# Optimization experiments

Measured on AMD Instinct MI355X. Metric: run time of the kernel, lower is better.

The kernel has to match this reference:

```python
import jax, jax.numpy as jnp
import numpy as np

N = 384       # nodes
K = 60        # neighbors per node
SUB = 20      # subsample_k
C_S = 128
C_Z = 128
H = 4
D_HEAD = C_Z // H
NUM_RBF = 64
E = N * K
EPS = 1e-8


def _rbf(D, D_min=0.0, D_max=20.0, D_count=NUM_RBF):
    # radial basis expansion of distances: [..., ] -> [..., D_count]
    mu = jnp.linspace(D_min, D_max, D_count)
    sigma = (D_max - D_min) / D_count
    return jnp.exp(-(((D[..., None] - mu) / sigma) ** 2))


def setup_inputs() -> dict:
    key = jax.random.key(0)
    ks = jax.random.split(key, 16)
    f32 = jnp.float32
    inp = {
        "node_features": jax.random.normal(ks[0], (N, C_S), f32),
        "node_trans": jax.random.normal(ks[1], (N, 3), f32) * 5.0,
        "edge_features": jax.random.normal(ks[2], (E, C_Z), f32),
        "edge_index": jax.random.randint(ks[3], (2, E), 0, N),
        "subsample_idx": jax.random.randint(ks[4], (N, K, SUB), 0, K),
        # dist_bias_gate: Linear(2*c_s -> H)
        "W_gate": jax.random.normal(ks[5], (2 * C_S, H), f32) / np.sqrt(2 * C_S),
        "b_gate": jnp.zeros((H,), f32),
        # dist_bias: Linear(num_rbf -> H)
        "W_db": jax.random.normal(ks[6], (NUM_RBF, H), f32) / np.sqrt(NUM_RBF),
        "b_db": jnp.zeros((H,), f32),
        # lin_qk: Linear(c_z -> 2*c_z)
        "W_qk": jax.random.normal(ks[7], (C_Z, 2 * C_Z), f32) / np.sqrt(C_Z),
        "b_qk": jnp.zeros((2 * C_Z,), f32),
        # lin_v: Linear(c_z -> c_z)
        "W_v": jax.random.normal(ks[8], (C_Z, C_Z), f32) / np.sqrt(C_Z),
        "b_v": jnp.zeros((C_Z,), f32),
        # lin_out: Linear(c_z -> c_z) (init='final' in source; random here for testing)
        "W_out": jax.random.normal(ks[9], (C_Z, C_Z), f32) / np.sqrt(C_Z),
        "b_out": jnp.zeros((C_Z,), f32),
    }
    return inp


def reference(node_features, node_trans, edge_features, edge_index, subsample_idx,
              W_gate, b_gate, W_db, b_db, W_qk, b_qk, W_v, b_v, W_out, b_out):
    n, k, sub = subsample_idx.shape
    # assume_sorted=True path: edges are grouped k-per-destination-node
    dst = edge_index[0].reshape(n, k)                           # [n,k] neighbor ids
    edge1 = jnp.broadcast_to(dst[:, :, None], (n, k, sub))      # [n,k,sub]
    edge2 = jnp.take_along_axis(
        jnp.broadcast_to(dst[:, None, :], (n, k, k)), subsample_idx, axis=-1)  # [n,k,sub]

    f1 = node_features[edge1]                                   # [n,k,sub,c_s]
    f2 = node_features[edge2]
    gate = jax.nn.sigmoid(jnp.concatenate([f1, f2], axis=-1) @ W_gate + b_gate)  # [n,k,sub,H]

    t1 = node_trans[edge1]                                      # [n,k,sub,3]
    t2 = node_trans[edge2]
    dist = jnp.linalg.norm(t1 - t2 + EPS, axis=-1)              # [n,k,sub]
    bias = gate * (_rbf(dist) @ W_db + b_db)                    # [n,k,sub,H]

    edges = edge_features.reshape(n, k, C_Z)
    qk = edges @ W_qk + b_qk
    q, kk = jnp.split(qk, 2, axis=-1)
    q = q.reshape(n, k, H, D_HEAD)
    kk = kk.reshape(n, k, H, D_HEAD)

    batch = jnp.arange(n)[:, None, None]
    k_sub = kk[batch, subsample_idx]                            # [n,k,sub,H,d]
    attn = jnp.einsum('nkhd,nkshd->nksh', q, k_sub) / np.sqrt(C_Z) + bias
    attn = jax.nn.softmax(attn, axis=2)                         # softmax over subsample axis

    v = (edges @ W_v + b_v).reshape(n, k, H, D_HEAD)
    v_sub = v[batch, subsample_idx]                             # [n,k,sub,H,d]
    upd = jnp.einsum('nksh,nkshd->nkhd', attn, v_sub).reshape(n * k, C_Z)
    return upd @ W_out + b_out                                  # [E, c_z]
```

## Files before the change

kernel.cpp:

```cpp
#include <hip/hip_runtime.h>
#include <hip/hip_bf16.h>

typedef unsigned short ushortT;
typedef __attribute__((ext_vector_type(8))) short bf16x8;
typedef __attribute__((ext_vector_type(4))) float f32x4;

#define N_NODES 384
#define KNBR 60
#define SUBK 20
#define NEDGE (N_NODES * KNBR)
#define EPSC 1e-8f
#define INV_SQRT_CZ 0.08838834764831845f
#define MU_STEP (20.0f / 63.0f)
#define INV_MU_STEP (63.0f / 20.0f)
#define INV_SIGMA 3.2f

__device__ __forceinline__ float bflo(unsigned int u) { return __uint_as_float(u << 16); }
__device__ __forceinline__ float bfhi(unsigned int u) { return __uint_as_float(u & 0xffff0000u); }
__device__ __forceinline__ ushortT f2bu(float v) {
  union { float f; unsigned int u; } c;
  c.f = v;
  return (ushortT)((c.u + 0x7fffu + ((c.u >> 16) & 1u)) >> 16);
}
__device__ __forceinline__ unsigned int pack2bf(float x, float y) {
  return (unsigned int)f2bu(x) | ((unsigned int)f2bu(y) << 16);
}
__device__ __forceinline__ ushortT f2h(float x) {
  _Float16 h = (_Float16)x;
  return __builtin_bit_cast(ushortT, h);
}
__device__ __forceinline__ float h2f(ushortT u) {
  return (float)__builtin_bit_cast(_Float16, u);
}

__global__ __launch_bounds__(256) void prep_kernel(
    const float* __restrict__ nf, const float* __restrict__ Wg, float* __restrict__ g,
    const float* __restrict__ Wqk, const float* __restrict__ bqk,
    const float* __restrict__ Wv, const float* __restrict__ bv,
    const float* __restrict__ Wout,
    ushortT* __restrict__ Wp1, ushortT* __restrict__ Wp2, float* __restrict__ bc) {
  int b = blockIdx.x, tid = threadIdx.x;
  if (b < 96) {
    int n = b * 4 + (tid >> 6), t = tid & 63;
    float a = nf[n * 128 + t];
    float bb = nf[n * 128 + 64 + t];
    float acc[8];
#pragma unroll
    for (int h = 0; h < 4; ++h) {
      acc[h]     = a * Wg[t * 4 + h]         + bb * Wg[(t + 64) * 4 + h];
      acc[4 + h] = a * Wg[(128 + t) * 4 + h] + bb * Wg[(192 + t) * 4 + h];
    }
#pragma unroll
    for (int i = 0; i < 8; ++i)
#pragma unroll
      for (int off = 32; off >= 1; off >>= 1) acc[i] += __shfl_xor(acc[i], off, 64);
    if (t == 0) {
#pragma unroll
      for (int i = 0; i < 8; ++i) g[n * 8 + i] = acc[i];
    }
  } else {
    int i = (b - 96) * 256 + tid;
    if (i < 49152) {
      int j = i & 7, l = (i >> 3) & 63, t = (i >> 9) & 3;
      int nt = (i >> 11) % 12, ny = (i >> 11) / 12;
      int nn = ny * 192 + nt * 16 + (l & 15);
      int k = t * 32 + (l >> 4) * 8 + j;
      float v = (nn < 256) ? Wqk[k * 256 + nn] : Wv[k * 128 + (nn - 256)];
      if (nn < 128) v *= INV_SQRT_CZ;
      Wp1[i] = f2bu(v);
    } else {
      int i2 = i - 49152;
      int j = i2 & 7, l = (i2 >> 3) & 63, t = (i2 >> 9) & 3, nt = (i2 >> 11);
      int nn = nt * 16 + (l & 15);
      int k = t * 32 + (l >> 4) * 8 + j;
      Wp2[i2] = f2bu(Wout[k * 128 + nn]);
    }
    if (i < 384) {
      float v = (i < 256) ? bqk[i] : bv[i - 256];
      if (i < 128) v *= INV_SQRT_CZ;
      bc[i] = v;
    }
  }
}

__global__ __launch_bounds__(512, 4) void fused_kernel(
    const float* __restrict__ ef, const ushortT* __restrict__ Wp1,
    const ushortT* __restrict__ Wp2, const float* __restrict__ bc,
    const float* __restrict__ bout, const float* __restrict__ g,
    const float* __restrict__ node_trans, const int* __restrict__ edge_index,
    const int* __restrict__ sub_idx, const float* __restrict__ W_db,
    const float* __restrict__ b_db, const float* __restrict__ b_gate,
    float* __restrict__ outp) {
  __shared__ __align__(16) ushortT kvb[KNBR * 256];
  __shared__ __align__(16) ushortT updq[64 * 136];
  __shared__ __align__(16) ushortT biasb[KNBR * SUBK * 4];
  __shared__ ushortT sub_lds[KNBR * SUBK];
  __shared__ float trs[KNBR * 3];
  __shared__ float gg[KNBR * 8];

  int n = blockIdx.x, tid = threadIdx.x;
  int e0 = n * KNBR;
  int w = tid >> 6, l = tid & 63;
  int lr = l & 15, lc = l >> 4;
  int rowA = (w & 3) * 16 + lr;
  int rowAc = min(rowA, KNBR - 1);
  int Tbase = (tid >> 8) * 12;

  if (tid < KNBR) {
    int dst = edge_index[e0 + tid];
#pragma unroll
    for (int c = 0; c < 3; ++c) trs[tid * 3 + c] = node_trans[dst * 3 + c];
#pragma unroll
    for (int i = 0; i < 8; ++i) gg[tid * 8 + i] = g[dst * 8 + i];
  }

  bf16x8 bcur[4], bnxt[4];
#pragma unroll
  for (int t = 0; t < 4; ++t)
    bcur[t] = *(const bf16x8*)(Wp1 + ((Tbase * 4 + t) * 64 + l) * 8);

  bf16x8 afrag[4];
#pragma unroll
  for (int t = 0; t < 4; ++t) {
    const float* ap = ef + (size_t)(e0 + rowAc) * 128 + t * 32 + lc * 8;
    float4 lo = *(const float4*)ap;
    float4 hi = *(const float4*)(ap + 4);
    bf16x8 a;
    a[0] = (short)f2bu(lo.x); a[1] = (short)f2bu(lo.y);
    a[2] = (short)f2bu(lo.z); a[3] = (short)f2bu(lo.w);
    a[4] = (short)f2bu(hi.x); a[5] = (short)f2bu(hi.y);
    a[6] = (short)f2bu(hi.z); a[7] = (short)f2bu(hi.w);
    afrag[t] = a;
  }

#pragma unroll
  for (int Ti = 0; Ti < 12; ++Ti) {
    int T = Tbase + Ti;
    if (Ti < 11) {
#pragma unroll
      for (int t = 0; t < 4; ++t)
        bnxt[t] = *(const bf16x8*)(Wp1 + (((T + 1) * 4 + t) * 64 + l) * 8);
    }
    f32x4 acc = {0.f, 0.f, 0.f, 0.f};
#pragma unroll
    for (int t = 0; t < 4; ++t)
      acc = __builtin_amdgcn_mfma_f32_16x16x32_bf16(bcur[t], afrag[t], acc, 0, 0, 0);
    int col0 = T * 16 + lc * 4;
    float4 bi = *(const float4*)(bc + col0);
    float o0 = acc[0] + bi.x, o1 = acc[1] + bi.y;
    float o2 = acc[2] + bi.z, o3 = acc[3] + bi.w;
    uint2 o;
    o.x = pack2bf(o0, o1);
    o.y = pack2bf(o2, o3);
    if (T < 8) {
      *(uint2*)(updq + rowA * 136 + col0) = o;
    } else if (rowA < KNBR) {
      int colk = col0 - 128;
      int base_b = (colk & 128) << 1;
      int d = colk & 127;
      int inner = ((d >> 3) & 1) * 128 + (((d >> 4) * 16) ^ ((rowA & 7) << 4)) + (d & 7) * 2;
      *(uint2*)((char*)kvb + rowA * 512 + base_b + inner) = o;
    }
#pragma unroll
    for (int t = 0; t < 4; ++t) bcur[t] = bnxt[t];
  }
  __syncthreads();

  float4 bgv = *(const float4*)b_gate;
  float4 bdbv = *(const float4*)b_db;
  for (int p = tid; p < KNBR * SUBK; p += 512) {
    int kl = p / SUBK, s = p - kl * SUBK;
    int j = sub_idx[(size_t)(e0 + kl) * SUBK + s];
    sub_lds[p] = (ushortT)j;
    float dx = trs[kl * 3 + 0] - trs[j * 3 + 0] + EPSC;
    float dy = trs[kl * 3 + 1] - trs[j * 3 + 1] + EPSC;
    float dz = trs[kl * 3 + 2] - trs[j * 3 + 2] + EPSC;
    float dist = sqrtf(dx * dx + dy * dy + dz * dz);
    int r0 = (int)(dist * INV_MU_STEP + 0.5f);
    int rlo = max(r0 - 4, 0), rhi = min(r0 + 4, 63);
    float a0 = 0.f, a1 = 0.f, a2 = 0.f, a3 = 0.f;
    for (int r = rlo; r <= rhi; ++r) {
      float t = (dist - r * MU_STEP) * INV_SIGMA;
      float e = __expf(-t * t);
      float4 wv = ((const float4*)W_db)[r];
      a0 += e * wv.x; a1 += e * wv.y; a2 += e * wv.z; a3 += e * wv.w;
    }
    float g1 = gg[kl * 8 + 0] + gg[j * 8 + 4 + 0] + bgv.x;
    float g2 = gg[kl * 8 + 1] + gg[j * 8 + 4 + 1] + bgv.y;
    float g3 = gg[kl * 8 + 2] + gg[j * 8 + 4 + 2] + bgv.z;
    float g4 = gg[kl * 8 + 3] + gg[j * 8 + 4 + 3] + bgv.w;
    biasb[p * 4 + 0] = f2h((a0 + bdbv.x) / (1.0f + __expf(-g1)));
    biasb[p * 4 + 1] = f2h((a1 + bdbv.y) / (1.0f + __expf(-g2)));
    biasb[p * 4 + 2] = f2h((a2 + bdbv.z) / (1.0f + __expf(-g3)));
    biasb[p * 4 + 3] = f2h((a3 + bdbv.w) / (1.0f + __expf(-g4)));
  }
  __syncthreads();

  int row3 = tid >> 3, h = (tid >> 1) & 3, dh = tid & 1;
  int row3c = min(row3, KNBR - 1);
  int hdo = (h * 2 + dh) * 16;
  const char* kvbase = (const char*)kvb;
  float q0, q1, q2, q3, q4, q5, q6, q7, q8, q9, q10, q11, q12, q13, q14, q15;
  {
    const ushortT* qp = updq + row3 * 136 + h * 32 + dh * 16;
    uint4 u0 = *(const uint4*)qp;
    uint4 u1 = *(const uint4*)(qp + 8);
    q0 = bflo(u0.x); q1 = bfhi(u0.x); q2 = bflo(u0.y); q3 = bfhi(u0.y);
    q4 = bflo(u0.z); q5 = bfhi(u0.z); q6 = bflo(u0.w); q7 = bfhi(u0.w);
    q8 = bflo(u1.x); q9 = bfhi(u1.x); q10 = bflo(u1.y); q11 = bfhi(u1.y);
    q12 = bflo(u1.z); q13 = bfhi(u1.z); q14 = bflo(u1.w); q15 = bfhi(u1.w);
  }
  float den = 0.f;
  float v0 = 0.f, v1 = 0.f, v2 = 0.f, v3 = 0.f, v4 = 0.f, v5 = 0.f, v6 = 0.f, v7 = 0.f;
  float v8 = 0.f, v9 = 0.f, v10 = 0.f, v11 = 0.f, v12 = 0.f, v13 = 0.f, v14 = 0.f, v15 = 0.f;
#pragma unroll 4
  for (int s = 0; s < SUBK; ++s) {
    int j = sub_lds[row3c * SUBK + s];
    int off = hdo ^ ((j & 7) << 4);
    const char* kr = kvbase + j * 512;
    uint4 k0 = *(const uint4*)(kr + off);
    uint4 k1 = *(const uint4*)(kr + 128 + off);
    float dot = q0 * bflo(k0.x) + q1 * bfhi(k0.x) + q2 * bflo(k0.y) + q3 * bfhi(k0.y) +
                q4 * bflo(k0.z) + q5 * bfhi(k0.z) + q6 * bflo(k0.w) + q7 * bfhi(k0.w) +
                q8 * bflo(k1.x) + q9 * bfhi(k1.x) + q10 * bflo(k1.y) + q11 * bfhi(k1.y) +
                q12 * bflo(k1.z) + q13 * bfhi(k1.z) + q14 * bflo(k1.w) + q15 * bfhi(k1.w);
    dot += __shfl_xor(dot, 1);
    float p = __expf(dot + h2f(biasb[(row3c * SUBK + s) * 4 + h]));
    den += p;
    uint4 w0 = *(const uint4*)(kr + 256 + off);
    uint4 w1 = *(const uint4*)(kr + 384 + off);
    v0 += p * bflo(w0.x); v1 += p * bfhi(w0.x); v2 += p * bflo(w0.y); v3 += p * bfhi(w0.y);
    v4 += p * bflo(w0.z); v5 += p * bfhi(w0.z); v6 += p * bflo(w0.w); v7 += p * bfhi(w0.w);
    v8 += p * bflo(w1.x); v9 += p * bfhi(w1.x); v10 += p * bflo(w1.y); v11 += p * bfhi(w1.y);
    v12 += p * bflo(w1.z); v13 += p * bfhi(w1.z); v14 += p * bflo(w1.w); v15 += p * bfhi(w1.w);
  }
  float inv = 1.0f / den;
  {
    uint4 o;
    o.x = pack2bf(v0 * inv, v1 * inv);
    o.y = pack2bf(v2 * inv, v3 * inv);
    o.z = pack2bf(v4 * inv, v5 * inv);
    o.w = pack2bf(v6 * inv, v7 * inv);
    *(uint4*)(updq + row3 * 136 + h * 32 + dh * 16) = o;
    uint4 o2;
    o2.x = pack2bf(v8 * inv, v9 * inv);
    o2.y = pack2bf(v10 * inv, v11 * inv);
    o2.z = pack2bf(v12 * inv, v13 * inv);
    o2.w = pack2bf(v14 * inv, v15 * inv);
    *(uint4*)(updq + row3 * 136 + h * 32 + dh * 16 + 8) = o2;
  }
  __syncthreads();

  int T4base = (tid >> 8) * 4;
  bf16x8 af2[4];
#pragma unroll
  for (int t = 0; t < 4; ++t)
    af2[t] = *(const bf16x8*)(updq + rowA * 136 + t * 32 + lc * 8);
  bf16x8 c2[4], n2[4];
#pragma unroll
  for (int t = 0; t < 4; ++t)
    c2[t] = *(const bf16x8*)(Wp2 + ((T4base * 4 + t) * 64 + l) * 8);
#pragma unroll
  for (int Ti = 0; Ti < 4; ++Ti) {
    int T = T4base + Ti;
    if (Ti < 3) {
#pragma unroll
      for (int t = 0; t < 4; ++t)
        n2[t] = *(const bf16x8*)(Wp2 + (((T + 1) * 4 + t) * 64 + l) * 8);
    }
    f32x4 acc = {0.f, 0.f, 0.f, 0.f};
#pragma unroll
    for (int t = 0; t < 4; ++t)
      acc = __builtin_amdgcn_mfma_f32_16x16x32_bf16(c2[t], af2[t], acc, 0, 0, 0);
    if (rowA < KNBR) {
      int col0 = T * 16 + lc * 4;
      float4 bi = *(const float4*)(bout + col0);
      float4 o;
      o.x = acc[0] + bi.x; o.y = acc[1] + bi.y;
      o.z = acc[2] + bi.z; o.w = acc[3] + bi.w;
      *(float4*)(outp + (size_t)(e0 + rowA) * 128 + col0) = o;
    }
#pragma unroll
    for (int t = 0; t < 4; ++t) c2[t] = n2[t];
  }
}

extern "C" void kernel_launch(void* const* d_in, const int* in_sizes, int n_in, void* d_out,
                              int out_size, void* d_ws, size_t ws_size, hipStream_t stream) {
  const float* nf  = (const float*)d_in[0];
  const float* nt  = (const float*)d_in[1];
  const float* ef  = (const float*)d_in[2];
  const int*   ei  = (const int*)d_in[3];
  const int*   si  = (const int*)d_in[4];
  const float* Wg  = (const float*)d_in[5];
  const float* bg  = (const float*)d_in[6];
  const float* Wdb = (const float*)d_in[7];
  const float* bdb = (const float*)d_in[8];
  const float* Wqk = (const float*)d_in[9];
  const float* bqk = (const float*)d_in[10];
  const float* Wv  = (const float*)d_in[11];
  const float* bv  = (const float*)d_in[12];
  const float* Wout = (const float*)d_in[13];
  const float* bout = (const float*)d_in[14];
  float* out = (float*)d_out;

  float* g      = (float*)d_ws;
  float* bc     = g + 3072;
  ushortT* Wp1  = (ushortT*)(bc + 384);
  ushortT* Wp2  = Wp1 + 49152;

  prep_kernel<<<dim3(352), dim3(256), 0, stream>>>(nf, Wg, g, Wqk, bqk, Wv, bv, Wout,
                                                   Wp1, Wp2, bc);
  fused_kernel<<<dim3(N_NODES), dim3(512), 0, stream>>>(ef, Wp1, Wp2, bc, bout, g, nt, ei, si,
                                                        Wdb, bdb, bg, out);
}
```

Before: 40.91 us.

## Vectorize attention dot/accumulate with float2 packed math and drop staging barrier

Rewrites the per-subsample QK dot product and PV accumulation using two-wide float vectors so the compiler can emit packed FMA instructions (v_pk_fma_f32) on CDNA. Separately, it removes the shared-memory staging of neighbor translations and gate terms, and the barrier that followed the first GEMM. The bias loop now reads edge_index, node_trans and g directly from global memory. This trades an LDS stage and a barrier for redundant, cache-served global gathers.

```diff
diff --git a/kernel.cpp b/kernel.cpp
--- a/kernel.cpp
+++ b/kernel.cpp
@@ -4,6 +4,7 @@
 typedef unsigned short ushortT;
 typedef __attribute__((ext_vector_type(8))) short bf16x8;
 typedef __attribute__((ext_vector_type(4))) float f32x4;
+typedef __attribute__((ext_vector_type(2))) float f32x2;
 
 #define N_NODES 384
 #define KNBR 60
@@ -17,6 +18,12 @@
 
 __device__ __forceinline__ float bflo(unsigned int u) { return __uint_as_float(u << 16); }
 __device__ __forceinline__ float bfhi(unsigned int u) { return __uint_as_float(u & 0xffff0000u); }
+__device__ __forceinline__ f32x2 bfpair(unsigned int u) {
+  f32x2 r;
+  r.x = bflo(u);
+  r.y = bfhi(u);
+  return r;
+}
 __device__ __forceinline__ ushortT f2bu(float v) {
   union { float f; unsigned int u; } c;
   c.f = v;
@@ -95,8 +102,6 @@
   __shared__ __align__(16) ushortT updq[64 * 136];
   __shared__ __align__(16) ushortT biasb[KNBR * SUBK * 4];
   __shared__ ushortT sub_lds[KNBR * SUBK];
-  __shared__ float trs[KNBR * 3];
-  __shared__ float gg[KNBR * 8];
 
   int n = blockIdx.x, tid = threadIdx.x;
   int e0 = n * KNBR;
@@ -105,14 +110,6 @@
   int rowA = (w & 3) * 16 + lr;
   int rowAc = min(rowA, KNBR - 1);
   int Tbase = (tid >> 8) * 12;
-
-  if (tid < KNBR) {
-    int dst = edge_index[e0 + tid];
-#pragma unroll
-    for (int c = 0; c < 3; ++c) trs[tid * 3 + c] = node_trans[dst * 3 + c];
-#pragma unroll
-    for (int i = 0; i < 8; ++i) gg[tid * 8 + i] = g[dst * 8 + i];
-  }
 
   bf16x8 bcur[4], bnxt[4];
 #pragma unroll
@@ -164,7 +161,6 @@
 #pragma unroll
     for (int t = 0; t < 4; ++t) bcur[t] = bnxt[t];
   }
-  __syncthreads();
 
   float4 bgv = *(const float4*)b_gate;
   float4 bdbv = *(const float4*)b_db;
@@ -172,9 +168,11 @@
     int kl = p / SUBK, s = p - kl * SUBK;
     int j = sub_idx[(size_t)(e0 + kl) * SUBK + s];
     sub_lds[p] = (ushortT)j;
-    float dx = trs[kl * 3 + 0] - trs[j * 3 + 0] + EPSC;
-    float dy = trs[kl * 3 + 1] - trs[j * 3 + 1] + EPSC;
-    float dz = trs[kl * 3 + 2] - trs[j * 3 + 2] + EPSC;
+    int dk = edge_index[e0 + kl];
+    int dj = edge_index[e0 + j];
+    float dx = node_trans[dk * 3 + 0] - node_trans[dj * 3 + 0] + EPSC;
+    float dy = node_trans[dk * 3 + 1] - node_trans[dj * 3 + 1] + EPSC;
+    float dz = node_trans[dk * 3 + 2] - node_trans[dj * 3 + 2] + EPSC;
     float dist = sqrtf(dx * dx + dy * dy + dz * dz);
     int r0 = (int)(dist * INV_MU_STEP + 0.5f);
     int rlo = max(r0 - 4, 0), rhi = min(r0 + 4, 63);
@@ -185,10 +183,12 @@
       float4 wv = ((const float4*)W_db)[r];
       a0 += e * wv.x; a1 += e * wv.y; a2 += e * wv.z; a3 += e * wv.w;
     }
-    float g1 = gg[kl * 8 + 0] + gg[j * 8 + 4 + 0] + bgv.x;
-    float g2 = gg[kl * 8 + 1] + gg[j * 8 + 4 + 1] + bgv.y;
-    float g3 = gg[kl * 8 + 2] + gg[j * 8 + 4 + 2] + bgv.z;
-    float g4 = gg[kl * 8 + 3] + gg[j * 8 + 4 + 3] + bgv.w;
+    float4 gk = *(const float4*)(g + dk * 8);
+    float4 gj = *(const float4*)(g + dj * 8 + 4);
+    float g1 = gk.x + gj.x + bgv.x;
+    float g2 = gk.y + gj.y + bgv.y;
+    float g3 = gk.z + gj.z + bgv.z;
+    float g4 = gk.w + gj.w + bgv.w;
     biasb[p * 4 + 0] = f2h((a0 + bdbv.x) / (1.0f + __expf(-g1)));
     biasb[p * 4 + 1] = f2h((a1 + bdbv.y) / (1.0f + __expf(-g2)));
     biasb[p * 4 + 2] = f2h((a2 + bdbv.z) / (1.0f + __expf(-g3)));
@@ -200,19 +200,17 @@
   int row3c = min(row3, KNBR - 1);
   int hdo = (h * 2 + dh) * 16;
   const char* kvbase = (const char*)kvb;
-  float q0, q1, q2, q3, q4, q5, q6, q7, q8, q9, q10, q11, q12, q13, q14, q15;
+  f32x2 qv0, qv1, qv2, qv3, qv4, qv5, qv6, qv7;
   {
     const ushortT* qp = updq + row3 * 136 + h * 32 + dh * 16;
     uint4 u0 = *(const uint4*)qp;
     uint4 u1 = *(const uint4*)(qp + 8);
-    q0 = bflo(u0.x); q1 = bfhi(u0.x); q2 = bflo(u0.y); q3 = bfhi(u0.y);
-    q4 = bflo(u0.z); q5 = bfhi(u0.z); q6 = bflo(u0.w); q7 = bfhi(u0.w);
-    q8 = bflo(u1.x); q9 = bfhi(u1.x); q10 = bflo(u1.y); q11 = bfhi(u1.y);
-    q12 = bflo(u1.z); q13 = bfhi(u1.z); q14 = bflo(u1.w); q15 = bfhi(u1.w);
+    qv0 = bfpair(u0.x); qv1 = bfpair(u0.y); qv2 = bfpair(u0.z); qv3 = bfpair(u0.w);
+    qv4 = bfpair(u1.x); qv5 = bfpair(u1.y); qv6 = bfpair(u1.z); qv7 = bfpair(u1.w);
   }
   float den = 0.f;
-  float v0 = 0.f, v1 = 0.f, v2 = 0.f, v3 = 0.f, v4 = 0.f, v5 = 0.f, v6 = 0.f, v7 = 0.f;
-  float v8 = 0.f, v9 = 0.f, v10 = 0.f, v11 = 0.f, v12 = 0.f, v13 = 0.f, v14 = 0.f, v15 = 0.f;
+  f32x2 va0 = {0.f, 0.f}, va1 = {0.f, 0.f}, va2 = {0.f, 0.f}, va3 = {0.f, 0.f};
+  f32x2 va4 = {0.f, 0.f}, va5 = {0.f, 0.f}, va6 = {0.f, 0.f}, va7 = {0.f, 0.f};
 #pragma unroll 4
   for (int s = 0; s < SUBK; ++s) {
     int j = sub_lds[row3c * SUBK + s];
@@ -220,33 +218,43 @@
     const char* kr = kvbase + j * 512;
     uint4 k0 = *(const uint4*)(kr + off);
     uint4 k1 = *(const uint4*)(kr + 128 + off);
-    float dot = q0 * bflo(k0.x) + q1 * bfhi(k0.x) + q2 * bflo(k0.y) + q3 * bfhi(k0.y) +
-                q4 * bflo(k0.z) + q5 * bfhi(k0.z) + q6 * bflo(k0.w) + q7 * bfhi(k0.w) +
-                q8 * bflo(k1.x) + q9 * bfhi(k1.x) + q10 * bflo(k1.y) + q11 * bfhi(k1.y) +
-                q12 * bflo(k1.z) + q13 * bfhi(k1.z) + q14 * bflo(k1.w) + q15 * bfhi(k1.w);
+    f32x2 dacc = qv0 * bfpair(k0.x);
+    dacc += qv1 * bfpair(k0.y);
+    dacc += qv2 * bfpair(k0.z);
+    dacc += qv3 * bfpair(k0.w);
+    dacc += qv4 * bfpair(k1.x);
+    dacc += qv5 * bfpair(k1.y);
+    dacc += qv6 * bfpair(k1.z);
+    dacc += qv7 * bfpair(k1.w);
+    float dot = dacc.x + dacc.y;
     dot += __shfl_xor(dot, 1);
     float p = __expf(dot + h2f(biasb[(row3c * SUBK + s) * 4 + h]));
     den += p;
+    f32x2 pp = {p, p};
     uint4 w0 = *(const uint4*)(kr + 256 + off);
     uint4 w1 = *(const uint4*)(kr + 384 + off);
-    v0 += p * bflo(w0.x); v1 += p * bfhi(w0.x); v2 += p * bflo(w0.y); v3 += p * bfhi(w0.y);
-    v4 += p * bflo(w0.z); v5 += p * bfhi(w0.z); v6 += p * bflo(w0.w); v7 += p * bfhi(w0.w);
-    v8 += p * bflo(w1.x); v9 += p * bfhi(w1.x); v10 += p * bflo(w1.y); v11 += p * bfhi(w1.y);
-    v12 += p * bflo(w1.z); v13 += p * bfhi(w1.z); v14 += p * bflo(w1.w); v15 += p * bfhi(w1.w);
+    va0 += pp * bfpair(w0.x);
+    va1 += pp * bfpair(w0.y);
+    va2 += pp * bfpair(w0.z);
+    va3 += pp * bfpair(w0.w);
+    va4 += pp * bfpair(w1.x);
+    va5 += pp * bfpair(w1.y);
+    va6 += pp * bfpair(w1.z);
+    va7 += pp * bfpair(w1.w);
   }
   float inv = 1.0f / den;
   {
     uint4 o;
-    o.x = pack2bf(v0 * inv, v1 * inv);
-    o.y = pack2bf(v2 * inv, v3 * inv);
-    o.z = pack2bf(v4 * inv, v5 * inv);
-    o.w = pack2bf(v6 * inv, v7 * inv);
+    o.x = pack2bf(va0.x * inv, va0.y * inv);
+    o.y = pack2bf(va1.x * inv, va1.y * inv);
+    o.z = pack2bf(va2.x * inv, va2.y * inv);
+    o.w = pack2bf(va3.x * inv, va3.y * inv);
     *(uint4*)(updq + row3 * 136 + h * 32 + dh * 16) = o;
     uint4 o2;
-    o2.x = pack2bf(v8 * inv, v9 * inv);
-    o2.y = pack2bf(v10 * inv, v11 * inv);
-    o2.z = pack2bf(v12 * inv, v13 * inv);
-    o2.w = pack2bf(v14 * inv, v15 * inv);
+    o2.x = pack2bf(va4.x * inv, va4.y * inv);
+    o2.y = pack2bf(va5.x * inv, va5.y * inv);
+    o2.z = pack2bf(va6.x * inv, va6.y * inv);
+    o2.w = pack2bf(va7.x * inv, va7.y * inv);
     *(uint4*)(updq + row3 * 136 + h * 32 + dh * 16 + 8) = o2;
   }
   __syncthreads();
```

Result: no change. 40.53 us (-0.9%).
